# Kernel optimization log

Measured on AMD Instinct MI355X. Metric: run time of the kernel, lower is better.

## Reference

```python
import jax, jax.numpy as jnp
import numpy as np

BATCH = 2048
TEMP = 0.5
EPS = 1e-12  # matches F.normalize default eps


def setup_inputs() -> dict:
    key = jax.random.key(0)
    k1, k2 = jax.random.split(key)
    emb_i = jax.random.normal(k1, (BATCH, 256), dtype=jnp.float32)
    emb_j = jax.random.normal(k2, (BATCH, 256), dtype=jnp.float32)
    return {"emb_i": emb_i, "emb_j": emb_j}


def _l2_normalize(x):
    norm = jnp.sqrt(jnp.sum(x * x, axis=1, keepdims=True))
    return x / jnp.maximum(norm, EPS)


def reference(emb_i, emb_j):
    n = emb_i.shape[0]  # = BATCH
    z_i = _l2_normalize(emb_i)
    z_j = _l2_normalize(emb_j)
    z = jnp.concatenate([z_i, z_j], axis=0)            # [2N, D]
    # cosine similarity of normalized vectors == plain GEMM
    sim = jnp.einsum('id,jd->ij', z, z)                # [2N, 2N]
    # positive pairs: diag offsets +N and -N
    sim_i_j = jnp.diagonal(sim, offset=n)              # [N]
    sim_j_i = jnp.diagonal(sim, offset=-n)             # [N]
    positives = jnp.concatenate([sim_i_j, sim_j_i])    # [2N]
    neg_mask = 1.0 - jnp.eye(2 * n, dtype=sim.dtype)   # [2N, 2N]
    numerator = jnp.exp(positives / TEMP)
    denominator = jnp.sum(neg_mask * jnp.exp(sim / TEMP), axis=1)  # [2N]
    loss_partial = -jnp.log(numerator / denominator)
    return jnp.sum(loss_partial) / (2 * n)
```

## Files before the change

### kernel.cpp

```cpp
#include <hip/hip_runtime.h>
#include <hip/hip_bf16.h>
#include <math.h>

#define NB        2048
#define TWO_N     4096
#define DIM       256
#define EPS       1e-12f
#define NT1D      (TWO_N / 128)
#define NTILES    (NT1D * (NT1D + 1) / 2)


typedef __attribute__((ext_vector_type(8))) short  bf16x8;
typedef __attribute__((ext_vector_type(4))) float  f32x4;

__global__ __launch_bounds__(256) void nrm_kernel(
    const float* __restrict__ emb_i, const float* __restrict__ emb_j,
    short* __restrict__ zt, float* __restrict__ pos,
    float* __restrict__ out)
{
    int t = threadIdx.x;
    int wave = t >> 6, lane = t & 63;
    int r = blockIdx.x * 4 + wave;
    float4 a = ((const float4*)(emb_i + (size_t)r * DIM))[lane];
    float4 b = ((const float4*)(emb_j + (size_t)r * DIM))[lane];
    float sa = a.x*a.x + a.y*a.y + a.z*a.z + a.w*a.w;
    float sb = b.x*b.x + b.y*b.y + b.z*b.z + b.w*b.w;
    float sd = a.x*b.x + a.y*b.y + a.z*b.z + a.w*b.w;
    #pragma unroll
    for (int off = 32; off >= 1; off >>= 1) {
        sa += __shfl_xor(sa, off, 64);
        sb += __shfl_xor(sb, off, 64);
        sd += __shfl_xor(sd, off, 64);
    }
    float si = 1.0f / fmaxf(sqrtf(sa), EPS);
    float sj = 1.0f / fmaxf(sqrtf(sb), EPS);

    int dst = (r >> 4) * 4096 + (lane >> 3) * 512 + ((lane >> 1) & 3) * 128
            + (r & 15) * 8 + (lane & 1) * 4;

    union { __hip_bfloat16 h[4]; uint2 u; } pk;
    pk.h[0] = __float2bfloat16(a.x * si);
    pk.h[1] = __float2bfloat16(a.y * si);
    pk.h[2] = __float2bfloat16(a.z * si);
    pk.h[3] = __float2bfloat16(a.w * si);
    *(uint2*)(zt + dst) = pk.u;
    pk.h[0] = __float2bfloat16(b.x * sj);
    pk.h[1] = __float2bfloat16(b.y * sj);
    pk.h[2] = __float2bfloat16(b.z * sj);
    pk.h[3] = __float2bfloat16(b.w * sj);
    *(uint2*)(zt + dst + 128 * 4096) = pk.u;

    if (lane == 0) pos[r] = sd * si * sj;
    if (blockIdx.x == 0 && t == 0) out[0] = 0.0f;
}

#define MFMA1(Av, Bv, m, n) \
    acc[m][n] = __builtin_amdgcn_mfma_f32_16x16x32_bf16(Av, Bv, acc[m][n], 0, 0, 0);

#define MFMA_ROW(Av, B0v, B1v, B2v, B3v, m) \
    MFMA1(Av, B0v, m, 0) MFMA1(Av, B1v, m, 1) \
    MFMA1(Av, B2v, m, 2) MFMA1(Av, B3v, m, 3)

#define MMSTEP(A0v, A1v, A2v, A3v, B0v, B1v, B2v, B3v) \
    MFMA_ROW(A0v, B0v, B1v, B2v, B3v, 0) \
    MFMA_ROW(A1v, B0v, B1v, B2v, B3v, 1) \
    MFMA_ROW(A2v, B0v, B1v, B2v, B3v, 2) \
    MFMA_ROW(A3v, B0v, B1v, B2v, B3v, 3)

#define SB __builtin_amdgcn_sched_barrier(0);

#define SLD(c) \
    G0 = *(const bf16x8*)(stg_base + 0 * 4096 + (2*(c)+0) * 512); \
    G1 = *(const bf16x8*)(stg_base + 0 * 4096 + (2*(c)+1) * 512); \
    G2 = *(const bf16x8*)(stg_base + 1 * 4096 + (2*(c)+0) * 512); \
    G3 = *(const bf16x8*)(stg_base + 1 * 4096 + (2*(c)+1) * 512); \
    G4 = *(const bf16x8*)(stg_base + 2 * 4096 + (2*(c)+0) * 512); \
    G5 = *(const bf16x8*)(stg_base + 2 * 4096 + (2*(c)+1) * 512); \
    G6 = *(const bf16x8*)(stg_base + 3 * 4096 + (2*(c)+0) * 512); \
    G7 = *(const bf16x8*)(stg_base + 3 * 4096 + (2*(c)+1) * 512);

#define DSW(bs) \
    *(bf16x8*)&lds[(bs)*16384 + (p0+0)*512 + l8] = G0; \
    *(bf16x8*)&lds[(bs)*16384 + (p0+1)*512 + l8] = G1; \
    *(bf16x8*)&lds[(bs)*16384 + (p0+2)*512 + l8] = G2; \
    *(bf16x8*)&lds[(bs)*16384 + (p0+3)*512 + l8] = G3; \
    *(bf16x8*)&lds[(bs)*16384 + (p0+4)*512 + l8] = G4; \
    *(bf16x8*)&lds[(bs)*16384 + (p0+5)*512 + l8] = G5; \
    *(bf16x8*)&lds[(bs)*16384 + (p0+6)*512 + l8] = G6; \
    *(bf16x8*)&lds[(bs)*16384 + (p0+7)*512 + l8] = G7;

#define CSTEP(bs, sl) \
    { \
        bf16x8 fa0 = *(const bf16x8*)&lds[(bs)*16384 + ((wm4+0)*2+(sl))*512 + l8]; \
        bf16x8 fa1 = *(const bf16x8*)&lds[(bs)*16384 + ((wm4+1)*2+(sl))*512 + l8]; \
        bf16x8 fa2 = *(const bf16x8*)&lds[(bs)*16384 + ((wm4+2)*2+(sl))*512 + l8]; \
        bf16x8 fa3 = *(const bf16x8*)&lds[(bs)*16384 + ((wm4+3)*2+(sl))*512 + l8]; \
        bf16x8 fb0 = *(const bf16x8*)&lds[(bs)*16384 + 8192 + ((wn4+0)*2+(sl))*512 + l8]; \
        bf16x8 fb1 = *(const bf16x8*)&lds[(bs)*16384 + 8192 + ((wn4+1)*2+(sl))*512 + l8]; \
        bf16x8 fb2 = *(const bf16x8*)&lds[(bs)*16384 + 8192 + ((wn4+2)*2+(sl))*512 + l8]; \
        bf16x8 fb3 = *(const bf16x8*)&lds[(bs)*16384 + 8192 + ((wn4+3)*2+(sl))*512 + l8]; \
        MMSTEP(fa0, fa1, fa2, fa3, fb0, fb1, fb2, fb3) \
    }

#define COMPUTE(bs) CSTEP(bs, 0) CSTEP(bs, 1)

__global__ __launch_bounds__(256, 2) void simexp_kernel(
    const short* __restrict__ zt, float* __restrict__ part)
{
    __shared__ short lds[2 * 16384];

    int id = blockIdx.x;
    int by = (int)((sqrtf(8.0f * (float)id + 1.0f) - 1.0f) * 0.5f);
    while ((by + 1) * (by + 2) / 2 <= id) ++by;
    while (by * (by + 1) / 2 > id) --by;
    int bx = id - by * (by + 1) / 2;

    int t = threadIdx.x;
    int w = t >> 6, lane = t & 63;
    int quad = lane >> 4, c16 = lane & 15;
    int wm = w >> 1, wn = w & 1;
    int wm4 = wm * 4, wn4 = wn * 4;
    int l8 = lane * 8;
    int p0 = w * 8;
    int rbase = bx * 128 + wm * 64;
    int jbase = by * 128 + wn * 64;

    const short* stg_base = zt
        + (size_t)((w < 2 ? bx : by) * 8 + (w & 1) * 4) * 4096 + l8;

    f32x4 acc[4][4];
    #pragma unroll
    for (int mt = 0; mt < 4; ++mt)
        #pragma unroll
        for (int nt = 0; nt < 4; ++nt)
            acc[mt][nt] = (f32x4){0.f, 0.f, 0.f, 0.f};

    bf16x8 G0, G1, G2, G3, G4, G5, G6, G7;

    SLD(0)
    DSW(0)
    __syncthreads();
    SLD(1) SB
    COMPUTE(0) SB
    DSW(1)
    __syncthreads();
    SLD(2) SB
    COMPUTE(1) SB
    DSW(0)
    __syncthreads();
    SLD(3) SB
    COMPUTE(0)   SB
    DSW(1)
    __syncthreads();
    COMPUTE(1)

    float rsum[4][4];
    #pragma unroll
    for (int mt = 0; mt < 4; ++mt)
        #pragma unroll
        for (int rg = 0; rg < 4; ++rg) rsum[mt][rg] = 0.f;

    if (bx == by) {
        #pragma unroll
        for (int mt = 0; mt < 4; ++mt) {
            #pragma unroll
            for (int nt = 0; nt < 4; ++nt) {
                int j = jbase + nt * 16 + c16;
                #pragma unroll
                for (int rg = 0; rg < 4; ++rg) {
                    int r = rbase + mt * 16 + quad * 4 + rg;
                    float e = __expf(2.0f * acc[mt][nt][rg]);
                    rsum[mt][rg] += (r == j) ? 0.f : e;
                }
            }
        }
    } else {
        float csum[4] = {0.f, 0.f, 0.f, 0.f};
        #pragma unroll
        for (int mt = 0; mt < 4; ++mt) {
            #pragma unroll
            for (int nt = 0; nt < 4; ++nt) {
                #pragma unroll
                for (int rg = 0; rg < 4; ++rg) {
                    float e = __expf(2.0f * acc[mt][nt][rg]);
                    rsum[mt][rg] += e;
                    csum[nt] += e;
                }
            }
        }
        #pragma unroll
        for (int nt = 0; nt < 4; ++nt) {
            float v = csum[nt];
            v += __shfl_xor(v, 16, 64);
            v += __shfl_xor(v, 32, 64);
            if (quad == 0)
                part[(size_t)(by * 128 + wn * 64 + nt * 16 + c16) * 64
                     + 2 * bx + wm] = v;
        }
    }

    #pragma unroll
    for (int mt = 0; mt < 4; ++mt) {
        #pragma unroll
        for (int rg = 0; rg < 4; ++rg) {
            float v = rsum[mt][rg];
            v += __shfl_xor(v, 1, 64);
            v += __shfl_xor(v, 2, 64);
            v += __shfl_xor(v, 4, 64);
            v += __shfl_xor(v, 8, 64);
            if (c16 == 0)
                part[(size_t)(rbase + mt * 16 + quad * 4 + rg) * 64
                     + 2 * by + wn] = v;
        }
    }
}

__global__ __launch_bounds__(128) void redloss_kernel(
    const float* __restrict__ part, const float* __restrict__ pos,
    float* __restrict__ out)
{
    int s = blockIdx.x, t = threadIdx.x;
    int r = s * 128 + t;
    const float4* p = (const float4*)(part + ((size_t)r << 6));
    float sum = 0.f;
    #pragma unroll
    for (int i = 0; i < 16; ++i) {
        float4 v = p[i];
        sum += v.x + v.y + v.z + v.w;
    }
    float val = logf(sum) - 2.0f * pos[r & (NB - 1)];
    #pragma unroll
    for (int off = 32; off >= 1; off >>= 1) val += __shfl_xor(val, off, 64);
    __shared__ float red[2];
    if ((t & 63) == 0) red[t >> 6] = val;
    __syncthreads();
    if (t == 0)
        atomicAdd(out, (red[0] + red[1]) * (1.0f / (float)TWO_N));
}

extern "C" void kernel_launch(void* const* d_in, const int* in_sizes, int n_in,
                              void* d_out, int out_size, void* d_ws, size_t ws_size,
                              hipStream_t stream)
{
    const float* emb_i = (const float*)d_in[0];
    const float* emb_j = (const float*)d_in[1];
    float* out = (float*)d_out;

    short* zt = (short*)d_ws;
    float* part = (float*)((char*)d_ws + (size_t)TWO_N * DIM * sizeof(short));
    float* pos = part + (size_t)TWO_N * 64;

    nrm_kernel<<<NB / 4, 256, 0, stream>>>(emb_i, emb_j, zt, pos, out);
    simexp_kernel<<<NTILES, 256, 0, stream>>>(zt, part);
    redloss_kernel<<<NT1D, 128, 0, stream>>>(part, pos, out);
}
```

Before: 76.89 us.

## Fuse three kernels into one cooperative kernel with grid-wide syncs

Merges the normalize, similarity-exp GEMM tile, and reduction kernels into a single cooperative launch of 512 blocks, with grid syncs between phases and a grid-stride loop over the 528 tiles. This removes two kernel-launch boundaries and their gaps. The cost is two grid barriers, a second tile pass for 16 blocks that leaves most of the GPU idle, and reliance on all 512 blocks being co-resident (two per CU at 256 CUs). The old three-kernel path remains as a fallback if the cooperative launch fails.

```diff
diff --git a/kernel.cpp b/kernel.cpp
--- a/kernel.cpp
+++ b/kernel.cpp
@@ -1,6 +1,9 @@
 #include <hip/hip_runtime.h>
+#include <hip/hip_cooperative_groups.h>
 #include <hip/hip_bf16.h>
 #include <math.h>
+
+namespace cg = cooperative_groups;
 
 #define NB        2048
 #define TWO_N     4096
@@ -8,19 +11,19 @@
 #define EPS       1e-12f
 #define NT1D      (TWO_N / 128)
 #define NTILES    (NT1D * (NT1D + 1) / 2)
+#define GRID      512
 
 
 typedef __attribute__((ext_vector_type(8))) short  bf16x8;
 typedef __attribute__((ext_vector_type(4))) float  f32x4;
 
-__global__ __launch_bounds__(256) void nrm_kernel(
+__device__ __forceinline__ void do_nrm(
     const float* __restrict__ emb_i, const float* __restrict__ emb_j,
-    short* __restrict__ zt, float* __restrict__ pos,
-    float* __restrict__ out)
-{
-    int t = threadIdx.x;
+    short* __restrict__ zt, float* __restrict__ pos, float* __restrict__ out,
+    int bid, int t)
+{
     int wave = t >> 6, lane = t & 63;
-    int r = blockIdx.x * 4 + wave;
+    int r = bid * 4 + wave;
     float4 a = ((const float4*)(emb_i + (size_t)r * DIM))[lane];
     float4 b = ((const float4*)(emb_j + (size_t)r * DIM))[lane];
     float sa = a.x*a.x + a.y*a.y + a.z*a.z + a.w*a.w;
@@ -51,7 +54,7 @@
     *(uint2*)(zt + dst + 128 * 4096) = pk.u;
 
     if (lane == 0) pos[r] = sd * si * sj;
-    if (blockIdx.x == 0 && t == 0) out[0] = 0.0f;
+    if (bid == 0 && t == 0) out[0] = 0.0f;
 }
 
 #define MFMA1(Av, Bv, m, n) \
@@ -104,18 +107,15 @@
 
 #define COMPUTE(bs) CSTEP(bs, 0) CSTEP(bs, 1)
 
-__global__ __launch_bounds__(256, 2) void simexp_kernel(
-    const short* __restrict__ zt, float* __restrict__ part)
-{
-    __shared__ short lds[2 * 16384];
-
-    int id = blockIdx.x;
+__device__ __forceinline__ void do_tile(
+    const short* __restrict__ zt, float* __restrict__ part,
+    short* lds, int id, int t)
+{
     int by = (int)((sqrtf(8.0f * (float)id + 1.0f) - 1.0f) * 0.5f);
     while ((by + 1) * (by + 2) / 2 <= id) ++by;
     while (by * (by + 1) / 2 > id) --by;
     int bx = id - by * (by + 1) / 2;
 
-    int t = threadIdx.x;
     int w = t >> 6, lane = t & 63;
     int quad = lane >> 4, c16 = lane & 15;
     int wm = w >> 1, wn = w & 1;
@@ -149,7 +149,7 @@
     DSW(0)
     __syncthreads();
     SLD(3) SB
-    COMPUTE(0)   SB
+    COMPUTE(0) SB
     DSW(1)
     __syncthreads();
     COMPUTE(1)
@@ -215,27 +215,71 @@
     }
 }
 
+__device__ __forceinline__ void do_red(
+    const float* __restrict__ part, const float* __restrict__ pos,
+    float* __restrict__ out, float* red, int s, int t)
+{
+    int r = s * 128 + t;
+    const float4* p = (const float4*)(part + ((size_t)r << 6));
+    float sum = 0.f;
+    #pragma unroll
+    for (int i = 0; i < 16; ++i) {
+        float4 v = p[i];
+        sum += v.x + v.y + v.z + v.w;
+    }
+    float val = logf(sum) - 2.0f * pos[r & (NB - 1)];
+    #pragma unroll
+    for (int off = 32; off >= 1; off >>= 1) val += __shfl_xor(val, off, 64);
+    if ((t & 63) == 0) red[t >> 6] = val;
+    __syncthreads();
+    if (t == 0)
+        atomicAdd(out, (red[0] + red[1]) * (1.0f / (float)TWO_N));
+}
+
+__global__ __launch_bounds__(256, 2) void fused_kernel(
+    const float* __restrict__ emb_i, const float* __restrict__ emb_j,
+    short* __restrict__ zt, float* __restrict__ part,
+    float* __restrict__ pos, float* __restrict__ out)
+{
+    __shared__ short lds[2 * 16384];
+    __shared__ float red[2];
+    int t = threadIdx.x, bid = blockIdx.x;
+
+    do_nrm(emb_i, emb_j, zt, pos, out, bid, t);
+
+    __threadfence();
+    cg::this_grid().sync();
+
+    for (int id = bid; id < NTILES; id += GRID)
+        do_tile(zt, part, lds, id, t);
+
+    __threadfence();
+    cg::this_grid().sync();
+
+    if (bid < 32 && t < 128)
+        do_red(part, pos, out, red, bid, t);
+}
+
+__global__ __launch_bounds__(256) void nrm_kernel(
+    const float* __restrict__ emb_i, const float* __restrict__ emb_j,
+    short* __restrict__ zt, float* __restrict__ pos, float* __restrict__ out)
+{
+    do_nrm(emb_i, emb_j, zt, pos, out, blockIdx.x, threadIdx.x);
+}
+
+__global__ __launch_bounds__(256, 2) void simexp_kernel(
+    const short* __restrict__ zt, float* __restrict__ part)
+{
+    __shared__ short lds[2 * 16384];
+    do_tile(zt, part, lds, blockIdx.x, threadIdx.x);
+}
+
 __global__ __launch_bounds__(128) void redloss_kernel(
     const float* __restrict__ part, const float* __restrict__ pos,
     float* __restrict__ out)
 {
-    int s = blockIdx.x, t = threadIdx.x;
-    int r = s * 128 + t;
-    const float4* p = (const float4*)(part + ((size_t)r << 6));
-    float sum = 0.f;
-    #pragma unroll
-    for (int i = 0; i < 16; ++i) {
-        float4 v = p[i];
-        sum += v.x + v.y + v.z + v.w;
-    }
-    float val = logf(sum) - 2.0f * pos[r & (NB - 1)];
-    #pragma unroll
-    for (int off = 32; off >= 1; off >>= 1) val += __shfl_xor(val, off, 64);
     __shared__ float red[2];
-    if ((t & 63) == 0) red[t >> 6] = val;
-    __syncthreads();
-    if (t == 0)
-        atomicAdd(out, (red[0] + red[1]) * (1.0f / (float)TWO_N));
+    do_red(part, pos, out, red, blockIdx.x, threadIdx.x);
 }
 
 extern "C" void kernel_launch(void* const* d_in, const int* in_sizes, int n_in,
@@ -250,7 +294,14 @@
     float* part = (float*)((char*)d_ws + (size_t)TWO_N * DIM * sizeof(short));
     float* pos = part + (size_t)TWO_N * 64;
 
-    nrm_kernel<<<NB / 4, 256, 0, stream>>>(emb_i, emb_j, zt, pos, out);
-    simexp_kernel<<<NTILES, 256, 0, stream>>>(zt, part);
-    redloss_kernel<<<NT1D, 128, 0, stream>>>(part, pos, out);
-}
+    void* args[] = { (void*)&emb_i, (void*)&emb_j, (void*)&zt,
+                     (void*)&part, (void*)&pos, (void*)&out };
+    hipError_t err = hipLaunchCooperativeKernel(
+        (const void*)fused_kernel, dim3(GRID), dim3(256), args, 0, stream);
+
+    if (err != hipSuccess) {
+        nrm_kernel<<<NB / 4, 256, 0, stream>>>(emb_i, emb_j, zt, pos, out);
+        simexp_kernel<<<NTILES, 256, 0, stream>>>(zt, part);
+        redloss_kernel<<<NT1D, 128, 0, stream>>>(part, pos, out);
+    }
+}
```

Result: slower. 287.8 us (+274.4%).

## Halve K-chunk per pipeline stage to shrink LDS and raise occupancy

Applied to the files above, without the earlier changes.

Splits the K=256 reduction into eight 32-wide stages instead of four 64-wide stages. Each stage now stages four bf16x8 vectors per thread instead of eight, which halves the LDS buffer and the staging registers. Launch bounds move from 2 to 3 blocks per CU to turn the freed resources into occupancy. In exchange there are twice as many block-wide barriers and less MFMA work between them to hide each global load.

```diff
diff --git a/kernel.cpp b/kernel.cpp
--- a/kernel.cpp
+++ b/kernel.cpp
@@ -70,44 +70,34 @@
 #define SB __builtin_amdgcn_sched_barrier(0);
 
 #define SLD(c) \
-    G0 = *(const bf16x8*)(stg_base + 0 * 4096 + (2*(c)+0) * 512); \
-    G1 = *(const bf16x8*)(stg_base + 0 * 4096 + (2*(c)+1) * 512); \
-    G2 = *(const bf16x8*)(stg_base + 1 * 4096 + (2*(c)+0) * 512); \
-    G3 = *(const bf16x8*)(stg_base + 1 * 4096 + (2*(c)+1) * 512); \
-    G4 = *(const bf16x8*)(stg_base + 2 * 4096 + (2*(c)+0) * 512); \
-    G5 = *(const bf16x8*)(stg_base + 2 * 4096 + (2*(c)+1) * 512); \
-    G6 = *(const bf16x8*)(stg_base + 3 * 4096 + (2*(c)+0) * 512); \
-    G7 = *(const bf16x8*)(stg_base + 3 * 4096 + (2*(c)+1) * 512);
+    G0 = *(const bf16x8*)(stg_base + 0 * 4096 + (c) * 512); \
+    G1 = *(const bf16x8*)(stg_base + 1 * 4096 + (c) * 512); \
+    G2 = *(const bf16x8*)(stg_base + 2 * 4096 + (c) * 512); \
+    G3 = *(const bf16x8*)(stg_base + 3 * 4096 + (c) * 512);
 
 #define DSW(bs) \
-    *(bf16x8*)&lds[(bs)*16384 + (p0+0)*512 + l8] = G0; \
-    *(bf16x8*)&lds[(bs)*16384 + (p0+1)*512 + l8] = G1; \
-    *(bf16x8*)&lds[(bs)*16384 + (p0+2)*512 + l8] = G2; \
-    *(bf16x8*)&lds[(bs)*16384 + (p0+3)*512 + l8] = G3; \
-    *(bf16x8*)&lds[(bs)*16384 + (p0+4)*512 + l8] = G4; \
-    *(bf16x8*)&lds[(bs)*16384 + (p0+5)*512 + l8] = G5; \
-    *(bf16x8*)&lds[(bs)*16384 + (p0+6)*512 + l8] = G6; \
-    *(bf16x8*)&lds[(bs)*16384 + (p0+7)*512 + l8] = G7;
-
-#define CSTEP(bs, sl) \
+    *(bf16x8*)&lds[(bs)*8192 + (p0+0)*512 + l8] = G0; \
+    *(bf16x8*)&lds[(bs)*8192 + (p0+1)*512 + l8] = G1; \
+    *(bf16x8*)&lds[(bs)*8192 + (p0+2)*512 + l8] = G2; \
+    *(bf16x8*)&lds[(bs)*8192 + (p0+3)*512 + l8] = G3;
+
+#define COMPUTE(bs) \
     { \
-        bf16x8 fa0 = *(const bf16x8*)&lds[(bs)*16384 + ((wm4+0)*2+(sl))*512 + l8]; \
-        bf16x8 fa1 = *(const bf16x8*)&lds[(bs)*16384 + ((wm4+1)*2+(sl))*512 + l8]; \
-        bf16x8 fa2 = *(const bf16x8*)&lds[(bs)*16384 + ((wm4+2)*2+(sl))*512 + l8]; \
-        bf16x8 fa3 = *(const bf16x8*)&lds[(bs)*16384 + ((wm4+3)*2+(sl))*512 + l8]; \
-        bf16x8 fb0 = *(const bf16x8*)&lds[(bs)*16384 + 8192 + ((wn4+0)*2+(sl))*512 + l8]; \
-        bf16x8 fb1 = *(const bf16x8*)&lds[(bs)*16384 + 8192 + ((wn4+1)*2+(sl))*512 + l8]; \
-        bf16x8 fb2 = *(const bf16x8*)&lds[(bs)*16384 + 8192 + ((wn4+2)*2+(sl))*512 + l8]; \
-        bf16x8 fb3 = *(const bf16x8*)&lds[(bs)*16384 + 8192 + ((wn4+3)*2+(sl))*512 + l8]; \
+        bf16x8 fa0 = *(const bf16x8*)&lds[(bs)*8192 + (wm4+0)*512 + l8]; \
+        bf16x8 fa1 = *(const bf16x8*)&lds[(bs)*8192 + (wm4+1)*512 + l8]; \
+        bf16x8 fa2 = *(const bf16x8*)&lds[(bs)*8192 + (wm4+2)*512 + l8]; \
+        bf16x8 fa3 = *(const bf16x8*)&lds[(bs)*8192 + (wm4+3)*512 + l8]; \
+        bf16x8 fb0 = *(const bf16x8*)&lds[(bs)*8192 + 4096 + (wn4+0)*512 + l8]; \
+        bf16x8 fb1 = *(const bf16x8*)&lds[(bs)*8192 + 4096 + (wn4+1)*512 + l8]; \
+        bf16x8 fb2 = *(const bf16x8*)&lds[(bs)*8192 + 4096 + (wn4+2)*512 + l8]; \
+        bf16x8 fb3 = *(const bf16x8*)&lds[(bs)*8192 + 4096 + (wn4+3)*512 + l8]; \
         MMSTEP(fa0, fa1, fa2, fa3, fb0, fb1, fb2, fb3) \
     }
 
-#define COMPUTE(bs) CSTEP(bs, 0) CSTEP(bs, 1)
-
-__global__ __launch_bounds__(256, 2) void simexp_kernel(
+__global__ __launch_bounds__(256, 3) void simexp_kernel(
     const short* __restrict__ zt, float* __restrict__ part)
 {
-    __shared__ short lds[2 * 16384];
+    __shared__ short lds[2 * 8192];
 
     int id = blockIdx.x;
     int by = (int)((sqrtf(8.0f * (float)id + 1.0f) - 1.0f) * 0.5f);
@@ -121,7 +111,7 @@
     int wm = w >> 1, wn = w & 1;
     int wm4 = wm * 4, wn4 = wn * 4;
     int l8 = lane * 8;
-    int p0 = w * 8;
+    int p0 = w * 4;
     int rbase = bx * 128 + wm * 64;
     int jbase = by * 128 + wn * 64;
 
@@ -135,22 +125,24 @@
         for (int nt = 0; nt < 4; ++nt)
             acc[mt][nt] = (f32x4){0.f, 0.f, 0.f, 0.f};
 
-    bf16x8 G0, G1, G2, G3, G4, G5, G6, G7;
+    bf16x8 G0, G1, G2, G3;
 
     SLD(0)
     DSW(0)
     __syncthreads();
-    SLD(1) SB
-    COMPUTE(0) SB
-    DSW(1)
-    __syncthreads();
-    SLD(2) SB
-    COMPUTE(1) SB
-    DSW(0)
-    __syncthreads();
-    SLD(3) SB
-    COMPUTE(0)   SB
-    DSW(1)
+    SLD(1) SB COMPUTE(0) SB DSW(1)
+    __syncthreads();
+    SLD(2) SB COMPUTE(1) SB DSW(0)
+    __syncthreads();
+    SLD(3) SB COMPUTE(0) SB DSW(1)
+    __syncthreads();
+    SLD(4) SB COMPUTE(1) SB DSW(0)
+    __syncthreads();
+    SLD(5) SB COMPUTE(0) SB DSW(1)
+    __syncthreads();
+    SLD(6) SB COMPUTE(1) SB DSW(0)
+    __syncthreads();
+    SLD(7) SB COMPUTE(0) SB DSW(1)
     __syncthreads();
     COMPUTE(1)
 
```

Result: faster. 74.13 us (-3.6%).
